# Kernel tuning notes

Hardware: AMD Instinct MI355X
Metric: run time of the kernel (lower is better)

## Reference

```python
import jax, jax.numpy as jnp
import numpy as np

TEMPERATURE = 0.07
EPS = 1e-8  # torch F.cosine_similarity default eps on the norm product


def setup_inputs() -> dict:
    key = jax.random.key(0)
    k1, k2 = jax.random.split(key)
    emb1 = jax.random.normal(k1, (8192, 128), dtype=jnp.float32)
    emb2 = jax.random.normal(k2, (8192, 128), dtype=jnp.float32)
    return {"emb1": emb1, "emb2": emb2}


def reference(emb1, emb2):
    B1 = emb1.shape[0]
    n1 = jnp.linalg.norm(emb1, axis=1)  # [B1]
    n2 = jnp.linalg.norm(emb2, axis=1)  # [B2]

    # Pairwise cosine similarities via GEMM + clamped norm product (matches F.cosine_similarity eps).
    sim11 = (emb1 @ emb1.T) / jnp.maximum(n1[:, None] * n1[None, :], EPS)  # [B1,B1]
    sim12 = (emb1 @ emb2.T) / jnp.maximum(n1[:, None] * n2[None, :], EPS)  # [B1,B2]

    # loss1 replicates the original loop: for i, for j in [i+1, B1): pair (i, (i+j) % B1).
    I = jnp.arange(B1)[:, None]
    J = jnp.arange(B1)[None, :]
    K = (I + J) % B1                                   # gathered column index
    mask = J > I                                       # j in [i+1, B1)
    vals = jnp.take_along_axis(sim11, K, axis=1)       # sim11[i, (i+j)%B1]
    loss1 = jnp.sum(jnp.where(mask, jnp.exp(vals / TEMPERATURE), 0.0))

    # loss2: all cross pairs between emb1 and emb2.
    loss2 = jnp.sum(jnp.exp(sim12 / TEMPERATURE))

    return (-jnp.log(loss1 / loss2)).reshape(1)
```

## Files before the change

kernel.cpp:

```cpp
#include <hip/hip_runtime.h>

#define B_ROWS   8192
#define BMASK    8191
#define DIM      128
#define BLK64    16384
#define NBLOCKS  1024

typedef __attribute__((ext_vector_type(8)))  __bf16 bf16x8;
typedef __attribute__((ext_vector_type(16))) float  f32x16;

#define RBSCALE 4.5398159f

__global__ __launch_bounds__(256)
void prep_kernel(const float* __restrict__ e1, const float* __restrict__ e2,
                 char* __restrict__ p1, char* __restrict__ p2,
                 float* __restrict__ acc) {
    if (blockIdx.x == 0 && threadIdx.x < 4) acc[threadIdx.x] = 0.f;
    const int rb = blockIdx.x;
    const float* src; char* dst; int rb_loc;
    if (rb < 128) { src = e1; dst = p1; rb_loc = rb; }
    else          { src = e2; dst = p2; rb_loc = rb - 128; }

    const int t  = threadIdx.x;
    const int rr = t >> 2;
    const int q  = t & 3;

    const float* rp = src + (size_t)(rb_loc * 64 + rr) * DIM + q * 32;
    float4 f[8];
    float ss = 0.f;
#pragma unroll
    for (int j = 0; j < 8; ++j) {
        f[j] = ((const float4*)rp)[j];
        ss += f[j].x * f[j].x + f[j].y * f[j].y + f[j].z * f[j].z + f[j].w * f[j].w;
    }
    ss += __shfl_xor(ss, 1);
    ss += __shfl_xor(ss, 2);
    const float rbn = RBSCALE / sqrtf(ss);

    char* db = dst + (size_t)rb_loc * BLK64;
#pragma unroll
    for (int j = 0; j < 4; ++j) {
        bf16x8 v;
        float4 a = f[2 * j], b = f[2 * j + 1];
        v[0] = (__bf16)(a.x * rbn); v[1] = (__bf16)(a.y * rbn);
        v[2] = (__bf16)(a.z * rbn); v[3] = (__bf16)(a.w * rbn);
        v[4] = (__bf16)(b.x * rbn); v[5] = (__bf16)(b.y * rbn);
        v[6] = (__bf16)(b.z * rbn); v[7] = (__bf16)(b.w * rbn);
        *(bf16x8*)(db + (size_t)(q * 4 + j) * 1024 + (size_t)rr * 16) = v;
    }
}

template <bool MASKED>
__device__ __forceinline__ float tile_sum(const f32x16& a0, const f32x16& a1,
                                          int i00, int c) {
    float s = 0.f;
#pragma unroll
    for (int g = 0; g < 2; ++g) {
        const f32x16& a = g ? a1 : a0;
        int ib = i00 + g * 32;
#pragma unroll
        for (int r = 0; r < 16; ++r) {
            float ev = exp2f(a[r]);
            if (MASKED) {
                int i = ib + (r & 3) + 8 * (r >> 2);
                int d = (c - i) & BMASK;
                s += (d > i) ? ev : 0.f;
            } else {
                s += ev;
            }
        }
    }
    return s;
}

__global__ __launch_bounds__(256, 3)
void pair_kernel(const char* __restrict__ P1, const char* __restrict__ P2,
                 float* __restrict__ accg, float* __restrict__ out) {
    __shared__ __align__(16) __bf16 Bbuf[2][8192];
    __shared__ float red[2][4];

    const int tid = threadIdx.x;
    const int b   = blockIdx.x;
    const int p   = b & 63;
    const int s   = b >> 6;

    const int i0  = 128 * p;
    const int e1  = (i0 > 128) ? i0 : 128;
    const int cnt = (p < 2) ? 128 : (130 - 2 * p);

    int n0 = cnt - 8 * s;
    n0 = (n0 < 0) ? 0 : ((n0 > 8) ? 8 : n0);
    const int L = n0 + 8;

    auto tile_src = [&](int m) -> const char* { return (m < n0) ? P1 : P2; };
    auto tile_c0  = [&](int m) -> int {
        if (m < n0) {
            int k = 8 * s + m;
            int e = (k == 0) ? 64 : e1 + 64 * (k - 1);
            return (i0 + e) & BMASK;
        }
        return 64 * (8 * s + (m - n0));
    };
    auto tile_masked = [&](int m) -> bool {
        if (m >= n0) return false;
        int k = 8 * s + m;
        int e = (k == 0) ? 64 : e1 + 64 * (k - 1);
        return (e < i0 + 256) || (e > 8128);
    };

    const int w  = tid >> 6, lane = tid & 63;
    const int w2 = w >> 1, wc = w & 1;
    const int l  = lane & 31, h = lane >> 5;

    bf16x8 af[2][8];
    {
        const char* ap = P1 + (size_t)(p * 2 + w2) * BLK64;
#pragma unroll
        for (int g = 0; g < 2; ++g)
#pragma unroll
            for (int sc = 0; sc < 8; ++sc)
                af[g][sc] = *(const bf16x8*)(ap + (size_t)(sc * 2 + h) * 1024
                                                + (size_t)(g * 32 + l) * 16);
    }

    auto stage = [&](int bufi, int m) {
        const char* gp = tile_src(m) + (size_t)(tile_c0(m) >> 6) * BLK64 + (size_t)tid * 16;
        char*       lp = (char*)&Bbuf[bufi][0] + (size_t)tid * 16;
#pragma unroll
        for (int r = 0; r < 4; ++r)
            __builtin_amdgcn_global_load_lds(
                (const __attribute__((address_space(1))) unsigned int*)(gp + r * 4096),
                (__attribute__((address_space(3))) unsigned int*)(lp + r * 4096),
                16, 0, 0);
    };

    const int i00 = i0 + w2 * 64 + 4 * h;
    const int cb  = wc * 32 + l;

    float s0 = 0.f, s1 = 0.f;
    stage(0, 0);
    int cur = 0;
    for (int m = 0; m < L; ++m) {
        __syncthreads();
        if (m + 1 < L) stage(cur ^ 1, m + 1);

        f32x16 a0, a1;
#pragma unroll
        for (int r = 0; r < 16; ++r) { a0[r] = 0.f; a1[r] = 0.f; }

        const char* bb = (const char*)&Bbuf[cur][0] + (size_t)cb * 16 + (size_t)h * 1024;
#pragma unroll
        for (int sc = 0; sc < 8; ++sc) {
            bf16x8 bf = *(const bf16x8*)(bb + (size_t)sc * 2048);
            a0 = __builtin_amdgcn_mfma_f32_32x32x16_bf16(af[0][sc], bf, a0, 0, 0, 0);
            a1 = __builtin_amdgcn_mfma_f32_32x32x16_bf16(af[1][sc], bf, a1, 0, 0, 0);
        }

        int c = tile_c0(m) + cb;
        float ts = tile_masked(m) ? tile_sum<true >(a0, a1, i00, c)
                                  : tile_sum<false>(a0, a1, i00, c);
        if (m < n0) s0 += ts; else s1 += ts;
        cur ^= 1;
    }

#pragma unroll
    for (int o = 32; o > 0; o >>= 1) {
        s0 += __shfl_down(s0, o);
        s1 += __shfl_down(s1, o);
    }
    if (lane == 0) { red[0][w] = s0; red[1][w] = s1; }
    __syncthreads();
    if (tid == 0) {
        atomicAdd(&accg[0], red[0][0] + red[0][1] + red[0][2] + red[0][3]);
        atomicAdd(&accg[1], red[1][0] + red[1][1] + red[1][2] + red[1][3]);
        __threadfence();
        unsigned prev = atomicAdd((unsigned*)&accg[2], 1u);
        if (prev == (unsigned)(NBLOCKS - 1)) {
            float l1 = atomicAdd(&accg[0], 0.f);
            float l2 = atomicAdd(&accg[1], 0.f);
            out[0] = -logf(l1 / l2);
        }
    }
}

extern "C" void kernel_launch(void* const* d_in, const int* in_sizes, int n_in,
                              void* d_out, int out_size, void* d_ws, size_t ws_size,
                              hipStream_t stream) {
    (void)in_sizes; (void)n_in; (void)out_size; (void)ws_size;
    const float* e1 = (const float*)d_in[0];
    const float* e2 = (const float*)d_in[1];
    float* out = (float*)d_out;
    char*  ws  = (char*)d_ws;

    float* acc = (float*)ws;
    char*  p1  = ws + 4096;
    char*  p2  = ws + 4096 + 2097152;

    prep_kernel<<<dim3(256), dim3(256), 0, stream>>>(e1, e2, p1, p2, acc);
    pair_kernel<<<dim3(NBLOCKS), dim3(256), 0, stream>>>(p1, p2, acc, out);
}
```

Measured before the change: 129.4 us.

## Fuse prep and pair kernels with grid barrier, enlarge row tile to 256

Merges the normalisation/bf16 conversion kernel into the pairwise kernel, using a global spin barrier on an atomic counter so all 384 persistent blocks wait until the packed data is ready. Each block now covers 256 rows with 4 accumulators per wave (64x64 per wave), which doubles reuse of each staged B tile. Work is split into 12 contiguous tile ranges per row block instead of fixed 8-tile chunks. Accumulators are zeroed with a memset before the launch. The grid barrier depends on all 384 blocks being co-resident (256 CUs at 2 blocks each), and the larger tile increases register pressure.

```diff
diff --git a/kernel.cpp b/kernel.cpp
--- a/kernel.cpp
+++ b/kernel.cpp
@@ -1,166 +1,163 @@
 #include <hip/hip_runtime.h>
 
-#define B_ROWS   8192
-#define BMASK    8191
-#define DIM      128
-#define BLK64    16384
-#define NBLOCKS  1024
+#define B_ROWS 8192
+#define BMASK  8191
+#define DIM    128
+#define BLK64  16384
+#define NB     384
 
 typedef __attribute__((ext_vector_type(8)))  __bf16 bf16x8;
 typedef __attribute__((ext_vector_type(16))) float  f32x16;
 
 #define RBSCALE 4.5398159f
 
-__global__ __launch_bounds__(256)
-void prep_kernel(const float* __restrict__ e1, const float* __restrict__ e2,
-                 char* __restrict__ p1, char* __restrict__ p2,
-                 float* __restrict__ acc) {
-    if (blockIdx.x == 0 && threadIdx.x < 4) acc[threadIdx.x] = 0.f;
-    const int rb = blockIdx.x;
-    const float* src; char* dst; int rb_loc;
-    if (rb < 128) { src = e1; dst = p1; rb_loc = rb; }
-    else          { src = e2; dst = p2; rb_loc = rb - 128; }
-
-    const int t  = threadIdx.x;
-    const int rr = t >> 2;
-    const int q  = t & 3;
-
-    const float* rp = src + (size_t)(rb_loc * 64 + rr) * DIM + q * 32;
-    float4 f[8];
-    float ss = 0.f;
-#pragma unroll
-    for (int j = 0; j < 8; ++j) {
-        f[j] = ((const float4*)rp)[j];
-        ss += f[j].x * f[j].x + f[j].y * f[j].y + f[j].z * f[j].z + f[j].w * f[j].w;
-    }
-    ss += __shfl_xor(ss, 1);
-    ss += __shfl_xor(ss, 2);
-    const float rbn = RBSCALE / sqrtf(ss);
-
-    char* db = dst + (size_t)rb_loc * BLK64;
-#pragma unroll
-    for (int j = 0; j < 4; ++j) {
-        bf16x8 v;
-        float4 a = f[2 * j], b = f[2 * j + 1];
-        v[0] = (__bf16)(a.x * rbn); v[1] = (__bf16)(a.y * rbn);
-        v[2] = (__bf16)(a.z * rbn); v[3] = (__bf16)(a.w * rbn);
-        v[4] = (__bf16)(b.x * rbn); v[5] = (__bf16)(b.y * rbn);
-        v[6] = (__bf16)(b.z * rbn); v[7] = (__bf16)(b.w * rbn);
-        *(bf16x8*)(db + (size_t)(q * 4 + j) * 1024 + (size_t)rr * 16) = v;
-    }
-}
-
-template <bool MASKED>
-__device__ __forceinline__ float tile_sum(const f32x16& a0, const f32x16& a1,
-                                          int i00, int c) {
-    float s = 0.f;
-#pragma unroll
-    for (int g = 0; g < 2; ++g) {
-        const f32x16& a = g ? a1 : a0;
-        int ib = i00 + g * 32;
-#pragma unroll
-        for (int r = 0; r < 16; ++r) {
-            float ev = exp2f(a[r]);
-            if (MASKED) {
-                int i = ib + (r & 3) + 8 * (r >> 2);
-                int d = (c - i) & BMASK;
-                s += (d > i) ? ev : 0.f;
-            } else {
-                s += ev;
-            }
-        }
-    }
-    return s;
-}
-
-__global__ __launch_bounds__(256, 3)
-void pair_kernel(const char* __restrict__ P1, const char* __restrict__ P2,
-                 float* __restrict__ accg, float* __restrict__ out) {
+__global__ __launch_bounds__(256, 2)
+void fused_kernel(const float* __restrict__ e1, const float* __restrict__ e2,
+                  char* __restrict__ P1, char* __restrict__ P2,
+                  float* __restrict__ acc, float* __restrict__ out) {
     __shared__ __align__(16) __bf16 Bbuf[2][8192];
     __shared__ float red[2][4];
 
     const int tid = threadIdx.x;
     const int b   = blockIdx.x;
-    const int p   = b & 63;
-    const int s   = b >> 6;
 
-    const int i0  = 128 * p;
-    const int e1  = (i0 > 128) ? i0 : 128;
-    const int cnt = (p < 2) ? 128 : (130 - 2 * p);
+    if (b < 256) {
+        const float* src; char* dst; int rb;
+        if (b < 128) { src = e1; dst = P1; rb = b; }
+        else         { src = e2; dst = P2; rb = b - 128; }
+        const int rr = tid >> 2, q = tid & 3;
+        const float* rp = src + (size_t)(rb * 64 + rr) * DIM + q * 32;
+        float4 f[8]; float ss = 0.f;
+#pragma unroll
+        for (int j = 0; j < 8; ++j) {
+            f[j] = ((const float4*)rp)[j];
+            ss += f[j].x*f[j].x + f[j].y*f[j].y + f[j].z*f[j].z + f[j].w*f[j].w;
+        }
+        ss += __shfl_xor(ss, 1); ss += __shfl_xor(ss, 2);
+        const float rs = RBSCALE / sqrtf(ss);
+        char* db = dst + (size_t)rb * BLK64;
+#pragma unroll
+        for (int j = 0; j < 4; ++j) {
+            bf16x8 v; float4 a = f[2*j], c = f[2*j+1];
+            v[0]=(__bf16)(a.x*rs); v[1]=(__bf16)(a.y*rs); v[2]=(__bf16)(a.z*rs); v[3]=(__bf16)(a.w*rs);
+            v[4]=(__bf16)(c.x*rs); v[5]=(__bf16)(c.y*rs); v[6]=(__bf16)(c.z*rs); v[7]=(__bf16)(c.w*rs);
+            *(bf16x8*)(db + (size_t)(q*4 + j)*1024 + (size_t)rr*16) = v;
+        }
+    }
 
-    int n0 = cnt - 8 * s;
-    n0 = (n0 < 0) ? 0 : ((n0 > 8) ? 8 : n0);
-    const int L = n0 + 8;
+    unsigned* spin = (unsigned*)(acc + 2);
+    __syncthreads();
+    if (tid == 0) {
+        __threadfence();
+        atomicAdd(spin, 1u);
+        while (__hip_atomic_load(spin, __ATOMIC_ACQUIRE, __HIP_MEMORY_SCOPE_AGENT) < NB)
+            __builtin_amdgcn_s_sleep(1);
+    }
+    __syncthreads();
+    __threadfence();
 
-    auto tile_src = [&](int m) -> const char* { return (m < n0) ? P1 : P2; };
-    auto tile_c0  = [&](int m) -> int {
-        if (m < n0) {
-            int k = 8 * s + m;
-            int e = (k == 0) ? 64 : e1 + 64 * (k - 1);
-            return (i0 + e) & BMASK;
+    const int p  = b & 31;
+    const int s  = b >> 5;
+    const int i0 = 256 * p;
+    const int mx  = (4 * p > 4) ? 4 * p : 4;
+    const int cnt = 132 - mx;
+    const int n_p = cnt + 128;
+    const int m_p = (n_p + 11) / 12;
+    const int t0  = s * m_p;
+    const int t1  = (t0 + m_p < n_p) ? (t0 + m_p) : n_p;
+
+    auto tile_info = [&](int t, int& c0, bool& msk, bool& isz0, const char*& src) {
+        if (t < cnt) {
+            int kk = (t < 3) ? (t + 1) : (mx + t - 3);
+            c0  = (i0 + 64 * kk) & BMASK;
+            msk = (kk <= 3) || (kk == 128) || (kk >= 4 * p && kk <= 4 * p + 7);
+            isz0 = true; src = P1;
+        } else {
+            c0 = 64 * (t - cnt); msk = false; isz0 = false; src = P2;
         }
-        return 64 * (8 * s + (m - n0));
-    };
-    auto tile_masked = [&](int m) -> bool {
-        if (m >= n0) return false;
-        int k = 8 * s + m;
-        int e = (k == 0) ? 64 : e1 + 64 * (k - 1);
-        return (e < i0 + 256) || (e > 8128);
     };
 
     const int w  = tid >> 6, lane = tid & 63;
-    const int w2 = w >> 1, wc = w & 1;
     const int l  = lane & 31, h = lane >> 5;
 
-    bf16x8 af[2][8];
-    {
-        const char* ap = P1 + (size_t)(p * 2 + w2) * BLK64;
+    float s0 = 0.f, s1 = 0.f;
+
+    if (t0 < t1) {
+        bf16x8 af[2][8];
+        {
+            const char* ap = P1 + (size_t)(4 * p + w) * BLK64;
 #pragma unroll
-        for (int g = 0; g < 2; ++g)
+            for (int g = 0; g < 2; ++g)
 #pragma unroll
-            for (int sc = 0; sc < 8; ++sc)
-                af[g][sc] = *(const bf16x8*)(ap + (size_t)(sc * 2 + h) * 1024
-                                                + (size_t)(g * 32 + l) * 16);
-    }
-
-    auto stage = [&](int bufi, int m) {
-        const char* gp = tile_src(m) + (size_t)(tile_c0(m) >> 6) * BLK64 + (size_t)tid * 16;
-        char*       lp = (char*)&Bbuf[bufi][0] + (size_t)tid * 16;
-#pragma unroll
-        for (int r = 0; r < 4; ++r)
-            __builtin_amdgcn_global_load_lds(
-                (const __attribute__((address_space(1))) unsigned int*)(gp + r * 4096),
-                (__attribute__((address_space(3))) unsigned int*)(lp + r * 4096),
-                16, 0, 0);
-    };
-
-    const int i00 = i0 + w2 * 64 + 4 * h;
-    const int cb  = wc * 32 + l;
-
-    float s0 = 0.f, s1 = 0.f;
-    stage(0, 0);
-    int cur = 0;
-    for (int m = 0; m < L; ++m) {
-        __syncthreads();
-        if (m + 1 < L) stage(cur ^ 1, m + 1);
-
-        f32x16 a0, a1;
-#pragma unroll
-        for (int r = 0; r < 16; ++r) { a0[r] = 0.f; a1[r] = 0.f; }
-
-        const char* bb = (const char*)&Bbuf[cur][0] + (size_t)cb * 16 + (size_t)h * 1024;
-#pragma unroll
-        for (int sc = 0; sc < 8; ++sc) {
-            bf16x8 bf = *(const bf16x8*)(bb + (size_t)sc * 2048);
-            a0 = __builtin_amdgcn_mfma_f32_32x32x16_bf16(af[0][sc], bf, a0, 0, 0, 0);
-            a1 = __builtin_amdgcn_mfma_f32_32x32x16_bf16(af[1][sc], bf, a1, 0, 0, 0);
+                for (int sc = 0; sc < 8; ++sc)
+                    af[g][sc] = *(const bf16x8*)(ap + (size_t)(sc * 2 + h) * 1024
+                                                    + (size_t)(g * 32 + l) * 16);
         }
 
-        int c = tile_c0(m) + cb;
-        float ts = tile_masked(m) ? tile_sum<true >(a0, a1, i00, c)
-                                  : tile_sum<false>(a0, a1, i00, c);
-        if (m < n0) s0 += ts; else s1 += ts;
-        cur ^= 1;
+        auto stage = [&](int bufi, int t) {
+            int c0; bool msk, isz0; const char* src;
+            tile_info(t, c0, msk, isz0, src);
+            const char* gp = src + (size_t)(c0 >> 6) * BLK64 + (size_t)tid * 16;
+            char*       lp = (char*)&Bbuf[bufi][0] + (size_t)tid * 16;
+#pragma unroll
+            for (int r = 0; r < 4; ++r)
+                __builtin_amdgcn_global_load_lds(
+                    (const __attribute__((address_space(1))) unsigned int*)(gp + r * 4096),
+                    (__attribute__((address_space(3))) unsigned int*)(lp + r * 4096),
+                    16, 0, 0);
+        };
+
+        const int i00 = i0 + 64 * w + 4 * h;
+
+        stage(0, t0);
+        int cur = 0;
+        for (int t = t0; t < t1; ++t) {
+            __syncthreads();
+            if (t + 1 < t1) stage(cur ^ 1, t + 1);
+
+            f32x16 a00, a01, a10, a11;
+#pragma unroll
+            for (int r = 0; r < 16; ++r) { a00[r] = 0.f; a01[r] = 0.f; a10[r] = 0.f; a11[r] = 0.f; }
+
+            const char* bb = (const char*)&Bbuf[cur][0] + (size_t)h * 1024 + (size_t)l * 16;
+#pragma unroll
+            for (int sc = 0; sc < 8; ++sc) {
+                bf16x8 b0 = *(const bf16x8*)(bb + (size_t)sc * 2048);
+                bf16x8 b1 = *(const bf16x8*)(bb + (size_t)sc * 2048 + 512);
+                a00 = __builtin_amdgcn_mfma_f32_32x32x16_bf16(af[0][sc], b0, a00, 0, 0, 0);
+                a01 = __builtin_amdgcn_mfma_f32_32x32x16_bf16(af[0][sc], b1, a01, 0, 0, 0);
+                a10 = __builtin_amdgcn_mfma_f32_32x32x16_bf16(af[1][sc], b0, a10, 0, 0, 0);
+                a11 = __builtin_amdgcn_mfma_f32_32x32x16_bf16(af[1][sc], b1, a11, 0, 0, 0);
+            }
+
+            int c0; bool msk, isz0; const char* src;
+            tile_info(t, c0, msk, isz0, src);
+
+            float ts = 0.f;
+            if (msk) {
+#pragma unroll
+                for (int g = 0; g < 2; ++g) {
+                    const f32x16& ac0 = g ? a10 : a00;
+                    const f32x16& ac1 = g ? a11 : a01;
+#pragma unroll
+                    for (int r = 0; r < 16; ++r) {
+                        int i = i00 + g * 32 + (r & 3) + 8 * (r >> 2);
+                        int c = c0 + l;
+                        int d = (c - i) & BMASK;
+                        ts += (d > i) ? exp2f(ac0[r]) : 0.f;
+                        int c2 = c + 32;
+                        int d2 = (c2 - i) & BMASK;
+                        ts += (d2 > i) ? exp2f(ac1[r]) : 0.f;
+                    }
+                }
+            } else {
+#pragma unroll
+                for (int r = 0; r < 16; ++r)
+                    ts += exp2f(a00[r]) + exp2f(a01[r]) + exp2f(a10[r]) + exp2f(a11[r]);
+            }
+            if (isz0) s0 += ts; else s1 += ts;
+            cur ^= 1;
+        }
     }
 
 #pragma unroll
@@ -171,13 +168,13 @@
     if (lane == 0) { red[0][w] = s0; red[1][w] = s1; }
     __syncthreads();
     if (tid == 0) {
-        atomicAdd(&accg[0], red[0][0] + red[0][1] + red[0][2] + red[0][3]);
-        atomicAdd(&accg[1], red[1][0] + red[1][1] + red[1][2] + red[1][3]);
+        atomicAdd(&acc[0], red[0][0] + red[0][1] + red[0][2] + red[0][3]);
+        atomicAdd(&acc[1], red[1][0] + red[1][1] + red[1][2] + red[1][3]);
         __threadfence();
-        unsigned prev = atomicAdd((unsigned*)&accg[2], 1u);
-        if (prev == (unsigned)(NBLOCKS - 1)) {
-            float l1 = atomicAdd(&accg[0], 0.f);
-            float l2 = atomicAdd(&accg[1], 0.f);
+        unsigned prev = atomicAdd((unsigned*)(acc + 3), 1u);
+        if (prev == (unsigned)(NB - 1)) {
+            float l1 = atomicAdd(&acc[0], 0.f);
+            float l2 = atomicAdd(&acc[1], 0.f);
             out[0] = -logf(l1 / l2);
         }
     }
@@ -196,6 +193,6 @@
     char*  p1  = ws + 4096;
     char*  p2  = ws + 4096 + 2097152;
 
-    prep_kernel<<<dim3(256), dim3(256), 0, stream>>>(e1, e2, p1, p2, acc);
-    pair_kernel<<<dim3(NBLOCKS), dim3(256), 0, stream>>>(p1, p2, acc, out);
+    hipMemsetAsync(acc, 0, 16, stream);
+    fused_kernel<<<dim3(NB), dim3(256), 0, stream>>>(e1, e2, p1, p2, acc, out);
 }
```

After: 197.3 us. +52.5%, slower.

## Balance 64x64 tiles evenly across waves with direct global B loads

Applied to the files above, without the earlier changes.

Replaces per-block band/segment scheduling with a flat list of 64x64 tiles split evenly across all waves. Each wave loads its own A band into registers and reads B fragments straight from global memory, dropping the LDS double buffer and block-wide barriers. The global atomic accumulators are spread over 32 slots to cut contention. In exchange there is no LDS reuse of B tiles across waves, so more global/L2 traffic, and occupancy is lowered to 2 blocks per SM.

```diff
diff --git a/kernel.cpp b/kernel.cpp
--- a/kernel.cpp
+++ b/kernel.cpp
@@ -1,21 +1,29 @@
 #include <hip/hip_runtime.h>
 
-#define B_ROWS   8192
-#define BMASK    8191
-#define DIM      128
-#define BLK64    16384
-#define NBLOCKS  1024
+#define B_ROWS 8192
+#define BMASK  8191
+#define DIM    128
+#define BLK64  16384
+#define NB     1024
+#define NWAVE  (NB * 4)
+#define NSLOT  32
+#define TTOT   24893
 
 typedef __attribute__((ext_vector_type(8)))  __bf16 bf16x8;
 typedef __attribute__((ext_vector_type(16))) float  f32x16;
 
 #define RBSCALE 4.5398159f
 
+__device__ __forceinline__ int qcount(int band) {
+    int m = (band < 2) ? 2 : band;
+    return 258 - m;
+}
+
 __global__ __launch_bounds__(256)
 void prep_kernel(const float* __restrict__ e1, const float* __restrict__ e2,
                  char* __restrict__ p1, char* __restrict__ p2,
                  float* __restrict__ acc) {
-    if (blockIdx.x == 0 && threadIdx.x < 4) acc[threadIdx.x] = 0.f;
+    if (blockIdx.x == 0 && threadIdx.x < 2 * NSLOT + 4) acc[threadIdx.x] = 0.f;
     const int rb = blockIdx.x;
     const float* src; char* dst; int rb_loc;
     if (rb < 128) { src = e1; dst = p1; rb_loc = rb; }
@@ -50,117 +58,95 @@
     }
 }
 
-template <bool MASKED>
-__device__ __forceinline__ float tile_sum(const f32x16& a0, const f32x16& a1,
-                                          int i00, int c) {
-    float s = 0.f;
-#pragma unroll
-    for (int g = 0; g < 2; ++g) {
-        const f32x16& a = g ? a1 : a0;
-        int ib = i00 + g * 32;
-#pragma unroll
-        for (int r = 0; r < 16; ++r) {
-            float ev = exp2f(a[r]);
-            if (MASKED) {
-                int i = ib + (r & 3) + 8 * (r >> 2);
-                int d = (c - i) & BMASK;
-                s += (d > i) ? ev : 0.f;
-            } else {
-                s += ev;
-            }
-        }
-    }
-    return s;
-}
-
-__global__ __launch_bounds__(256, 3)
+__global__ __launch_bounds__(256, 2)
 void pair_kernel(const char* __restrict__ P1, const char* __restrict__ P2,
-                 float* __restrict__ accg, float* __restrict__ out) {
-    __shared__ __align__(16) __bf16 Bbuf[2][8192];
+                 float* __restrict__ acc, float* __restrict__ out) {
     __shared__ float red[2][4];
 
-    const int tid = threadIdx.x;
-    const int b   = blockIdx.x;
-    const int p   = b & 63;
-    const int s   = b >> 6;
+    const int tid  = threadIdx.x;
+    const int b    = blockIdx.x;
+    const int w    = tid >> 6, lane = tid & 63;
+    const int l    = lane & 31, h = lane >> 5;
+    const int W    = b * 4 + w;
 
-    const int i0  = 128 * p;
-    const int e1  = (i0 > 128) ? i0 : 128;
-    const int cnt = (p < 2) ? 128 : (130 - 2 * p);
+    const int t_start = (int)(((long long)W       * TTOT) / NWAVE);
+    const int t_end   = (int)(((long long)(W + 1) * TTOT) / NWAVE);
 
-    int n0 = cnt - 8 * s;
-    n0 = (n0 < 0) ? 0 : ((n0 > 8) ? 8 : n0);
-    const int L = n0 + 8;
-
-    auto tile_src = [&](int m) -> const char* { return (m < n0) ? P1 : P2; };
-    auto tile_c0  = [&](int m) -> int {
-        if (m < n0) {
-            int k = 8 * s + m;
-            int e = (k == 0) ? 64 : e1 + 64 * (k - 1);
-            return (i0 + e) & BMASK;
-        }
-        return 64 * (8 * s + (m - n0));
-    };
-    auto tile_masked = [&](int m) -> bool {
-        if (m >= n0) return false;
-        int k = 8 * s + m;
-        int e = (k == 0) ? 64 : e1 + 64 * (k - 1);
-        return (e < i0 + 256) || (e > 8128);
-    };
-
-    const int w  = tid >> 6, lane = tid & 63;
-    const int w2 = w >> 1, wc = w & 1;
-    const int l  = lane & 31, h = lane >> 5;
-
-    bf16x8 af[2][8];
-    {
-        const char* ap = P1 + (size_t)(p * 2 + w2) * BLK64;
-#pragma unroll
-        for (int g = 0; g < 2; ++g)
-#pragma unroll
-            for (int sc = 0; sc < 8; ++sc)
-                af[g][sc] = *(const bf16x8*)(ap + (size_t)(sc * 2 + h) * 1024
-                                                + (size_t)(g * 32 + l) * 16);
-    }
-
-    auto stage = [&](int bufi, int m) {
-        const char* gp = tile_src(m) + (size_t)(tile_c0(m) >> 6) * BLK64 + (size_t)tid * 16;
-        char*       lp = (char*)&Bbuf[bufi][0] + (size_t)tid * 16;
-#pragma unroll
-        for (int r = 0; r < 4; ++r)
-            __builtin_amdgcn_global_load_lds(
-                (const __attribute__((address_space(1))) unsigned int*)(gp + r * 4096),
-                (__attribute__((address_space(3))) unsigned int*)(lp + r * 4096),
-                16, 0, 0);
-    };
-
-    const int i00 = i0 + w2 * 64 + 4 * h;
-    const int cb  = wc * 32 + l;
+    int band = 0, rem = t_start;
+    while (rem >= qcount(band)) { rem -= qcount(band); ++band; }
 
     float s0 = 0.f, s1 = 0.f;
-    stage(0, 0);
-    int cur = 0;
-    for (int m = 0; m < L; ++m) {
-        __syncthreads();
-        if (m + 1 < L) stage(cur ^ 1, m + 1);
+    bf16x8 af[2][8];
+    bool need_a = true;
 
-        f32x16 a0, a1;
+    for (int t = t_start; t < t_end; ++t) {
+        const int i0  = 64 * band;
+        const int mx  = (band < 2) ? 2 : band;
+        const int cnt0 = 130 - mx;
+
+        if (need_a) {
+            const char* ap = P1 + (size_t)band * BLK64;
 #pragma unroll
-        for (int r = 0; r < 16; ++r) { a0[r] = 0.f; a1[r] = 0.f; }
+            for (int g = 0; g < 2; ++g)
+#pragma unroll
+                for (int sc = 0; sc < 8; ++sc)
+                    af[g][sc] = *(const bf16x8*)(ap + (size_t)(sc * 2 + h) * 1024
+                                                    + (size_t)(g * 32 + l) * 16);
+            need_a = false;
+        }
 
-        const char* bb = (const char*)&Bbuf[cur][0] + (size_t)cb * 16 + (size_t)h * 1024;
+        const char* src; int c0; bool msk, isz0;
+        if (rem < cnt0) {
+            int e = (rem == 0) ? 64 : 64 * (mx + rem - 1);
+            c0   = (i0 + e) & BMASK;
+            msk  = (e < i0 + 128) || (e > B_ROWS - 64);
+            isz0 = true;  src = P1;
+        } else {
+            c0 = 64 * (rem - cnt0); msk = false; isz0 = false; src = P2;
+        }
+
+        const char* bp = src + (size_t)(c0 >> 6) * BLK64 + (size_t)h * 1024 + (size_t)l * 16;
+
+        f32x16 a00, a01, a10, a11;
+#pragma unroll
+        for (int r = 0; r < 16; ++r) { a00[r] = 0.f; a01[r] = 0.f; a10[r] = 0.f; a11[r] = 0.f; }
+
 #pragma unroll
         for (int sc = 0; sc < 8; ++sc) {
-            bf16x8 bf = *(const bf16x8*)(bb + (size_t)sc * 2048);
-            a0 = __builtin_amdgcn_mfma_f32_32x32x16_bf16(af[0][sc], bf, a0, 0, 0, 0);
-            a1 = __builtin_amdgcn_mfma_f32_32x32x16_bf16(af[1][sc], bf, a1, 0, 0, 0);
+            bf16x8 b0 = *(const bf16x8*)(bp + (size_t)sc * 2048);
+            bf16x8 b1 = *(const bf16x8*)(bp + (size_t)sc * 2048 + 512);
+            a00 = __builtin_amdgcn_mfma_f32_32x32x16_bf16(af[0][sc], b0, a00, 0, 0, 0);
+            a01 = __builtin_amdgcn_mfma_f32_32x32x16_bf16(af[0][sc], b1, a01, 0, 0, 0);
+            a10 = __builtin_amdgcn_mfma_f32_32x32x16_bf16(af[1][sc], b0, a10, 0, 0, 0);
+            a11 = __builtin_amdgcn_mfma_f32_32x32x16_bf16(af[1][sc], b1, a11, 0, 0, 0);
         }
 
-        int c = tile_c0(m) + cb;
-        float ts = tile_masked(m) ? tile_sum<true >(a0, a1, i00, c)
-                                  : tile_sum<false>(a0, a1, i00, c);
-        if (m < n0) s0 += ts; else s1 += ts;
-        cur ^= 1;
+        const int i00 = i0 + 4 * h;
+        float ts = 0.f;
+        if (msk) {
+#pragma unroll
+            for (int g = 0; g < 2; ++g) {
+                const f32x16& ac0 = g ? a10 : a00;
+                const f32x16& ac1 = g ? a11 : a01;
+#pragma unroll
+                for (int r = 0; r < 16; ++r) {
+                    int i  = i00 + g * 32 + (r & 3) + 8 * (r >> 2);
+                    int c  = c0 + l;
+                    int d  = (c - i) & BMASK;
+                    ts += (d > i) ? exp2f(ac0[r]) : 0.f;
+                    int c2 = c + 32;
+                    int d2 = (c2 - i) & BMASK;
+                    ts += (d2 > i) ? exp2f(ac1[r]) : 0.f;
+                }
+            }
+        } else {
+#pragma unroll
+            for (int r = 0; r < 16; ++r)
+                ts += exp2f(a00[r]) + exp2f(a01[r]) + exp2f(a10[r]) + exp2f(a11[r]);
+        }
+        if (isz0) s0 += ts; else s1 += ts;
+
+        if (++rem == qcount(band)) { rem = 0; ++band; need_a = true; }
     }
 
 #pragma unroll
@@ -171,13 +157,18 @@
     if (lane == 0) { red[0][w] = s0; red[1][w] = s1; }
     __syncthreads();
     if (tid == 0) {
-        atomicAdd(&accg[0], red[0][0] + red[0][1] + red[0][2] + red[0][3]);
-        atomicAdd(&accg[1], red[1][0] + red[1][1] + red[1][2] + red[1][3]);
+        int slot = b & (NSLOT - 1);
+        atomicAdd(&acc[slot],         red[0][0] + red[0][1] + red[0][2] + red[0][3]);
+        atomicAdd(&acc[NSLOT + slot], red[1][0] + red[1][1] + red[1][2] + red[1][3]);
         __threadfence();
-        unsigned prev = atomicAdd((unsigned*)&accg[2], 1u);
-        if (prev == (unsigned)(NBLOCKS - 1)) {
-            float l1 = atomicAdd(&accg[0], 0.f);
-            float l2 = atomicAdd(&accg[1], 0.f);
+        unsigned prev = atomicAdd((unsigned*)(acc + 2 * NSLOT), 1u);
+        if (prev == (unsigned)(NB - 1)) {
+            float l1 = 0.f, l2 = 0.f;
+#pragma unroll
+            for (int j = 0; j < NSLOT; ++j) {
+                l1 += __hip_atomic_load(&acc[j],         __ATOMIC_RELAXED, __HIP_MEMORY_SCOPE_AGENT);
+                l2 += __hip_atomic_load(&acc[NSLOT + j], __ATOMIC_RELAXED, __HIP_MEMORY_SCOPE_AGENT);
+            }
             out[0] = -logf(l1 / l2);
         }
     }
@@ -197,5 +188,5 @@
     char*  p2  = ws + 4096 + 2097152;
 
     prep_kernel<<<dim3(256), dim3(256), 0, stream>>>(e1, e2, p1, p2, acc);
-    pair_kernel<<<dim3(NBLOCKS), dim3(256), 0, stream>>>(p1, p2, acc, out);
+    pair_kernel<<<dim3(NB), dim3(256), 0, stream>>>(p1, p2, acc, out);
 }
```

Measured after the change: 120.9 us. 1.07x faster.
